# Performance work log

Hardware: AMD Instinct MI355X
Metric: run time of the kernel (lower is better)

## Reference

```python
import jax, jax.numpy as jnp
import numpy as np

N_TRAIN, D, N_EVAL, N_LABELS, K = 100000, 256, 2048, 100, 5


def setup_inputs() -> dict:
    key = jax.random.key(0)
    k1, k2, k3, k4 = jax.random.split(key, 4)
    X_train = jax.random.normal(k1, (N_TRAIN, D), dtype=jnp.float32)
    M = jax.random.normal(k2, (D, D), dtype=jnp.float32)
    X_eval = jax.random.normal(k3, (N_EVAL, D), dtype=jnp.float32)
    y_train = jax.random.randint(k4, (N_TRAIN,), 0, N_LABELS, dtype=jnp.int64 if jax.config.jax_enable_x64 else jnp.int32)
    return {"X_train": X_train, "M": M, "X_eval": X_eval, "y_train": y_train, "n_neighbors": K}


def reference(X_train, M, X_eval, y_train, n_neighbors):
    # cache = X_train @ M (precomputed in the torch module's __init__)
    cache = X_train @ M                                   # [N_train, d]
    X_prod = jnp.sum(cache * X_train, axis=1)             # [N_train]
    Y_prod = jnp.sum((X_eval @ M) * X_eval, axis=1)       # [N_eval]
    cross = cache @ X_eval.T                              # [N_train, N_eval]
    csd = X_prod[:, None] + Y_prod[None, :] - 2.0 * cross # [N_train, N_eval]
    # smallest-k distances per eval point -> top_k of negated distances
    _, indices = jax.lax.top_k(-csd.T, n_neighbors)       # [N_eval, k]
    neighbor_labels = y_train[indices]                    # [N_eval, k]
    n_labels = N_LABELS
    counts = jax.nn.one_hot(neighbor_labels, n_labels, dtype=jnp.float32).sum(axis=1)  # [N_eval, n_labels]
    uniques = jnp.arange(n_labels, dtype=jnp.float32)
    eps = 1.0 / n_labels
    return counts - uniques[None, :] * eps
```

## Files before the change

kernel.cpp:

```cpp
#include <hip/hip_runtime.h>
#include <cfloat>
#include <cstdint>


#define DD    256
#define NLAB  100
#define KNN   5
#define BCOLS 64
#define CHUNK 4224
#define NSRC  8

typedef float4 f4;
typedef __attribute__((ext_vector_type(8))) short bfrag;
typedef __attribute__((ext_vector_type(4))) float f32x4;

__device__ __forceinline__ void gload_lds16(const void* g, void* l) {
  __builtin_amdgcn_global_load_lds(
      (const __attribute__((address_space(1))) void*)g,
      (__attribute__((address_space(3))) void*)l, 16, 0, 0);
}

__device__ __forceinline__ uint32_t hi16(float v) {
  return ((__float_as_uint(v) + 0x8000u) & 0xffff0000u) >> 16;
}

__device__ __forceinline__ void split3(float v, uint32_t& h, uint32_t& m, uint32_t& l) {
  uint32_t b = __float_as_uint(v);
  uint32_t hb = (b + 0x8000u) & 0xffff0000u;
  float r1 = v - __uint_as_float(hb);
  uint32_t b1 = __float_as_uint(r1);
  uint32_t mb = (b1 + 0x8000u) & 0xffff0000u;
  float r2 = r1 - __uint_as_float(mb);
  uint32_t lb = (__float_as_uint(r2) + 0x8000u) & 0xffff0000u;
  h = hb >> 16; m = mb >> 16; l = lb >> 16;
}

__device__ __forceinline__ bool lex_lt(float v, int id, float rv, int rid) {
  return (v < rv) || (v == rv && id < rid);
}

__device__ __forceinline__ void ins5run(float (&bv)[KNN], int (&bi)[KNN], float v, int id) {
  if (v < bv[4]) {
    if (v < bv[3]) {
      bv[4] = bv[3]; bi[4] = bi[3];
      if (v < bv[2]) {
        bv[3] = bv[2]; bi[3] = bi[2];
        if (v < bv[1]) {
          bv[2] = bv[1]; bi[2] = bi[1];
          if (v < bv[0]) {
            bv[1] = bv[0]; bi[1] = bi[0]; bv[0] = v; bi[0] = id;
          } else { bv[1] = v; bi[1] = id; }
        } else { bv[2] = v; bi[2] = id; }
      } else { bv[3] = v; bi[3] = id; }
    } else { bv[4] = v; bi[4] = id; }
  }
}

__device__ __forceinline__ void ins5lex(float (&bv)[KNN], int (&bi)[KNN], float v, int id) {
  if (!lex_lt(v, id, bv[4], bi[4])) return;
  if (lex_lt(v, id, bv[3], bi[3])) {
    bv[4] = bv[3]; bi[4] = bi[3];
    if (lex_lt(v, id, bv[2], bi[2])) {
      bv[3] = bv[2]; bi[3] = bi[2];
      if (lex_lt(v, id, bv[1], bi[1])) {
        bv[2] = bv[1]; bi[2] = bi[1];
        if (lex_lt(v, id, bv[0], bi[0])) {
          bv[1] = bv[0]; bi[1] = bi[0]; bv[0] = v; bi[0] = id;
        } else { bv[1] = v; bi[1] = id; }
      } else { bv[2] = v; bi[2] = id; }
    } else { bv[3] = v; bi[3] = id; }
  } else { bv[4] = v; bi[4] = id; }
}

__device__ __forceinline__ void ins10(float (&bv)[10], int (&bi)[10], float v, int id) {
  if (!lex_lt(v, id, bv[9], bi[9])) return;
  bool placed = false;
#pragma unroll
  for (int s = 9; s >= 1; --s) {
    if (!placed) {
      if (lex_lt(v, id, bv[s - 1], bi[s - 1])) { bv[s] = bv[s - 1]; bi[s] = bi[s - 1]; }
      else { bv[s] = v; bi[s] = id; placed = true; }
    }
  }
  if (!placed) { bv[0] = v; bi[0] = id; }
}

__global__ __launch_bounds__(256)
void msplit_kernel(const float* __restrict__ M, uint4* __restrict__ MT3) {
  int id = blockIdx.x * 256 + threadIdx.x;
  int lane = id & 63;
  int nf = (id >> 6) & 15;
  int kit = id >> 10;
  int d = nf * 16 + (lane & 15);
  int kb = kit * 32 + (lane >> 4) * 8;
  uint32_t hw[4], mw[4], lw[4];
#pragma unroll
  for (int e = 0; e < 4; ++e) {
    uint32_t h0, m0, l0, h1, m1, l1;
    split3(M[(size_t)(kb + 2 * e) * DD + d], h0, m0, l0);
    split3(M[(size_t)(kb + 2 * e + 1) * DD + d], h1, m1, l1);
    hw[e] = h0 | (h1 << 16); mw[e] = m0 | (m1 << 16); lw[e] = l0 | (l1 << 16);
  }
  size_t base = (size_t)(kit * 16 + nf) * 3 * 64;
  MT3[base + lane]       = make_uint4(hw[0], hw[1], hw[2], hw[3]);
  MT3[base + 64 + lane]  = make_uint4(mw[0], mw[1], mw[2], mw[3]);
  MT3[base + 128 + lane] = make_uint4(lw[0], lw[1], lw[2], lw[3]);
}

__global__ __launch_bounds__(256)
void xsplit_kernel(const float* __restrict__ X, uint4* __restrict__ Xsp,
                   int NT, int NT128) {
  int id = blockIdx.x * 256 + threadIdx.x;
  int tile = id >> 12;
  if (tile >= NT128) return;
  int rem = id & 4095;
  int kit = rem >> 10;
  int s = rem & 1023;
  int m = s >> 3, pos = s & 7;
  int jj = pos ^ (m & 7);
  int row = tile * 128 + m; if (row >= NT) row = NT - 1;
  const float* src = X + (size_t)row * DD + kit * 64 + jj * 8;
  f4 v0 = *(const f4*)src;
  f4 v1 = *(const f4*)(src + 4);
  uint32_t h0 = hi16(v0.x) | (hi16(v0.y) << 16);
  uint32_t h1 = hi16(v0.z) | (hi16(v0.w) << 16);
  uint32_t h2 = hi16(v1.x) | (hi16(v1.y) << 16);
  uint32_t h3 = hi16(v1.z) | (hi16(v1.w) << 16);
  Xsp[(((size_t)tile * 4 + kit) << 10) + s] = make_uint4(h0, h1, h2, h3);
}

__global__ __launch_bounds__(256)
void prep_kernel(const float* __restrict__ M, const float* __restrict__ Xe,
                 float* __restrict__ ZTf32, uint4* __restrict__ Z2h, int NEVAL) {
  __shared__ float xe_lds[64 * 257];
  const int t = threadIdx.x;
  const int j0 = blockIdx.x * 64;
  const int part = t >> 6;
  const int dbase = blockIdx.y * 64 + part * 16;
#pragma unroll
  for (int it = 0; it < 16; ++it) {
    int id = t + it * 256;
    int r = id >> 6, k4 = id & 63;
    f4 v = *(const f4*)(Xe + (size_t)(j0 + r) * DD + 4 * k4);
    float* p = &xe_lds[r * 257 + 4 * k4];
    p[0] = v.x; p[1] = v.y; p[2] = v.z; p[3] = v.w;
  }
  __syncthreads();
  const int j = t & 63;
  float acc[16];
#pragma unroll
  for (int dd = 0; dd < 16; ++dd) acc[dd] = 0.f;
  for (int k4 = 0; k4 < 64; ++k4) {
    const float* xp = &xe_lds[j * 257 + 4 * k4];
    float x0 = xp[0], x1 = xp[1], x2 = xp[2], x3 = xp[3];
#pragma unroll
    for (int dd = 0; dd < 16; ++dd) {
      f4 m = *(const f4*)(M + (size_t)(dbase + dd) * DD + 4 * k4);
      acc[dd] = fmaf(m.x, x0, fmaf(m.y, x1, fmaf(m.z, x2, fmaf(m.w, x3, acc[dd]))));
    }
  }
  const int jg = j0 + j;
#pragma unroll
  for (int dd = 0; dd < 16; ++dd)
    ZTf32[(size_t)(dbase + dd) * NEVAL + jg] = acc[dd];
  const int cc = jg & 63, ct2 = jg >> 6;
  const int kit64 = dbase >> 6;
  const int jb = (dbase & 63) >> 3;
  size_t zbase = (size_t)ct2 * 2048 + kit64 * 512 + cc * 8;
#pragma unroll
  for (int u = 0; u < 2; ++u) {
    int jj = jb + u;
    uint32_t hw[4];
#pragma unroll
    for (int e = 0; e < 4; ++e) {
      uint32_t a0 = hi16(-2.f * acc[u * 8 + 2 * e]);
      uint32_t a1 = hi16(-2.f * acc[u * 8 + 2 * e + 1]);
      hw[e] = a0 | (a1 << 16);
    }
    Z2h[zbase + (jj ^ (cc & 7))] = make_uint4(hw[0], hw[1], hw[2], hw[3]);
  }
}

__global__ __launch_bounds__(256, 2)
void xprod_kernel(const float* __restrict__ X, const uint4* __restrict__ MT3,
                  float* __restrict__ Xprod, int NT) {
  __shared__ __align__(16) char pool[66560];
  short* A3 = (short*)pool;
  char*  B3 = pool + 12288;
  float* C  = (float*)pool;

  const int t = threadIdx.x;
  const int w = t >> 6, lane = t & 63;
  const int l15 = lane & 15, l4 = lane >> 4;
  const int row0 = blockIdx.x * 64;
  const int r = t >> 2, g = t & 3;
  int grow = row0 + r; if (grow >= NT) grow = NT - 1;
  const float* xrow = X + (size_t)grow * DD;

  f32x4 acc[16];
#pragma unroll
  for (int nf = 0; nf < 16; ++nf) { f32x4 z = {0.f, 0.f, 0.f, 0.f}; acc[nf] = z; }

  for (int kit = 0; kit < 8; ++kit) {
    f4 v0 = *(const f4*)(xrow + kit * 32 + g * 8);
    f4 v1 = *(const f4*)(xrow + kit * 32 + g * 8 + 4);
    uint32_t h[8], m[8], l[8];
    split3(v0.x, h[0], m[0], l[0]); split3(v0.y, h[1], m[1], l[1]);
    split3(v0.z, h[2], m[2], l[2]); split3(v0.w, h[3], m[3], l[3]);
    split3(v1.x, h[4], m[4], l[4]); split3(v1.y, h[5], m[5], l[5]);
    split3(v1.z, h[6], m[6], l[6]); split3(v1.w, h[7], m[7], l[7]);
    int slot = (r & 15) + 16 * g;
    int wb = r >> 4;
    *(uint4*)((char*)A3 + ((wb * 3 + 0) * 64 + slot) * 16) =
        make_uint4(h[0] | (h[1] << 16), h[2] | (h[3] << 16), h[4] | (h[5] << 16), h[6] | (h[7] << 16));
    *(uint4*)((char*)A3 + ((wb * 3 + 1) * 64 + slot) * 16) =
        make_uint4(m[0] | (m[1] << 16), m[2] | (m[3] << 16), m[4] | (m[5] << 16), m[6] | (m[7] << 16));
    *(uint4*)((char*)A3 + ((wb * 3 + 2) * 64 + slot) * 16) =
        make_uint4(l[0] | (l[1] << 16), l[2] | (l[3] << 16), l[4] | (l[5] << 16), l[6] | (l[7] << 16));
    const uint4* src = MT3 + (size_t)kit * 3072;
#pragma unroll
    for (int i = 0; i < 12; ++i) {
      int gs = (w * 12 + i) * 64;
      gload_lds16(src + gs + lane, B3 + (size_t)gs * 16);
    }
    __syncthreads();
    bfrag ah = *(const bfrag*)((const char*)A3 + ((w * 3 + 0) * 64 + lane) * 16);
    bfrag am = *(const bfrag*)((const char*)A3 + ((w * 3 + 1) * 64 + lane) * 16);
    bfrag al = *(const bfrag*)((const char*)A3 + ((w * 3 + 2) * 64 + lane) * 16);
#pragma unroll
    for (int nf = 0; nf < 16; ++nf) {
      bfrag bh = *(const bfrag*)(B3 + ((nf * 3 + 0) * 64 + lane) * 16);
      bfrag bm = *(const bfrag*)(B3 + ((nf * 3 + 1) * 64 + lane) * 16);
      bfrag bl = *(const bfrag*)(B3 + ((nf * 3 + 2) * 64 + lane) * 16);
      acc[nf] = __builtin_amdgcn_mfma_f32_16x16x32_bf16(ah, bh, acc[nf], 0, 0, 0);
      acc[nf] = __builtin_amdgcn_mfma_f32_16x16x32_bf16(ah, bm, acc[nf], 0, 0, 0);
      acc[nf] = __builtin_amdgcn_mfma_f32_16x16x32_bf16(am, bh, acc[nf], 0, 0, 0);
      acc[nf] = __builtin_amdgcn_mfma_f32_16x16x32_bf16(ah, bl, acc[nf], 0, 0, 0);
      acc[nf] = __builtin_amdgcn_mfma_f32_16x16x32_bf16(al, bh, acc[nf], 0, 0, 0);
      acc[nf] = __builtin_amdgcn_mfma_f32_16x16x32_bf16(am, bm, acc[nf], 0, 0, 0);
    }
    __syncthreads();
  }
#pragma unroll
  for (int nf = 0; nf < 16; ++nf)
#pragma unroll
    for (int reg = 0; reg < 4; ++reg)
      C[(size_t)(16 * w + l4 * 4 + reg) * 260 + nf * 16 + l15] = acc[nf][reg];
  __syncthreads();
  float part = 0.f;
#pragma unroll
  for (int j = 0; j < 16; ++j) {
    f4 xv = *(const f4*)(xrow + g * 64 + 4 * j);
    f4 cv = *(const f4*)&C[(size_t)r * 260 + g * 64 + 4 * j];
    part = fmaf(xv.x, cv.x, fmaf(xv.y, cv.y, fmaf(xv.z, cv.z, fmaf(xv.w, cv.w, part))));
  }
  part += __shfl_xor(part, 1);
  part += __shfl_xor(part, 2);
  if (g == 0 && row0 + r < NT) Xprod[row0 + r] = part;
}

__global__ __launch_bounds__(256, 3)
void cross_topk_kernel(const uint4* __restrict__ Xsp, const uint4* __restrict__ Z2h,
                       const float* __restrict__ Xprod,
                       float* __restrict__ cand_v, int* __restrict__ cand_i,
                       int NT, int NCH, int NT128) {
  __shared__ __align__(16) char Abuf[2][16384];
  __shared__ __align__(16) char Bbuf[2][8192];
  __shared__ __align__(16) float xp_lds[256];

  const int t = threadIdx.x;
  const int w = t >> 6, lane = t & 63;
  const int l15 = lane & 15, l4 = lane >> 4;
  const int wr = (w & 1) * 64;
  const int wc = (w >> 1) * 32;
  int n = blockIdx.y * gridDim.x + blockIdx.x;
  int nwg = gridDim.x * gridDim.y;
  int wg = n;
  if ((nwg & 7) == 0) wg = (n & 7) * (nwg >> 3) + (n >> 3);
  const int ct = wg % gridDim.x;
  const int ch = wg / gridDim.x;
  const int c0 = ct * BCOLS;
  const int row0 = ch * CHUNK;
  const int rows = min(CHUNK, NT - row0);
  const int nrp = (rows + 127) >> 7;
  const int G = nrp * 4;
  const int tile0 = ch * (CHUNK >> 7);

  float bv[2][KNN]; int bi[2][KNN];
#pragma unroll
  for (int nf = 0; nf < 2; ++nf)
#pragma unroll
    for (int s = 0; s < KNN; ++s) { bv[nf][s] = FLT_MAX; bi[nf][s] = 0x7fffffff; }

  f32x4 acc[4][2];
#pragma unroll
  for (int mf = 0; mf < 4; ++mf)
#pragma unroll
    for (int nf = 0; nf < 2; ++nf) { f32x4 z = {0.f, 0.f, 0.f, 0.f}; acc[mf][nf] = z; }

  auto stageA = [&](int gg) {
    int tile = tile0 + (gg >> 2); if (tile >= NT128) tile = NT128 - 1;
    const uint4* src = Xsp + (((size_t)tile * 4 + (gg & 3)) << 10);
    char* dst = Abuf[gg & 1];
#pragma unroll
    for (int i = 0; i < 4; ++i) {
      int sb = (w * 4 + i) * 64;
      gload_lds16(src + sb + lane, dst + sb * 16);
    }
  };
  auto stageB = [&](int gg) {
    const uint4* src = Z2h + (size_t)ct * 2048 + (gg & 3) * 512;
    char* dst = Bbuf[gg & 1];
#pragma unroll
    for (int i = 0; i < 2; ++i) {
      int sb = (w * 2 + i) * 64;
      gload_lds16(src + sb + lane, dst + sb * 16);
    }
  };

  stageA(0); stageB(0);
  asm volatile("s_waitcnt vmcnt(0)" ::: "memory");
  __builtin_amdgcn_s_barrier();

  for (int rp = 0; rp < nrp; ++rp) {
#pragma unroll
    for (int kit = 0; kit < 4; ++kit) {
      const int g = rp * 4 + kit;
      if (g < G - 1) {
        stageA(g + 1); stageB(g + 1);
        if (kit == 0 && !(rp & 1)) {
          gload_lds16((const uint4*)(Xprod + row0 + rp * 128) + lane,
                      (char*)xp_lds);
        }
        asm volatile("s_waitcnt vmcnt(3)" ::: "memory");
      } else {
        asm volatile("s_waitcnt vmcnt(0)" ::: "memory");
      }
      __builtin_amdgcn_s_barrier();
      const char* Ab = Abuf[kit & 1];
      const char* Bb = Bbuf[kit & 1];
      bfrag ah[4][2], bh[2][2];
#pragma unroll
      for (int mf = 0; mf < 4; ++mf) {
        int m = wr + mf * 16 + l15;
        const char* rb = Ab + m * 128;
#pragma unroll
        for (int ks = 0; ks < 2; ++ks)
          ah[mf][ks] = *(const bfrag*)(rb + (((ks * 4 + l4) ^ (m & 7)) << 4));
      }
#pragma unroll
      for (int nf = 0; nf < 2; ++nf) {
        int cc = wc + nf * 16 + l15;
        const char* rb = Bb + cc * 128;
#pragma unroll
        for (int ks = 0; ks < 2; ++ks)
          bh[nf][ks] = *(const bfrag*)(rb + (((ks * 4 + l4) ^ (cc & 7)) << 4));
      }
      __builtin_amdgcn_s_setprio(1);
#pragma unroll
      for (int ks = 0; ks < 2; ++ks)
#pragma unroll
        for (int mf = 0; mf < 4; ++mf)
#pragma unroll
          for (int nf = 0; nf < 2; ++nf)
            acc[mf][nf] = __builtin_amdgcn_mfma_f32_16x16x32_bf16(
                ah[mf][ks], bh[nf][ks], acc[mf][nf], 0, 0, 0);
      __builtin_amdgcn_s_setprio(0);
      if (kit == 3) {
        const int trow0 = row0 + rp * 128;
        const bool full = (trow0 + 128 <= NT);
#pragma unroll
        for (int mf = 0; mf < 4; ++mf) {
          f4 xv = *(const f4*)&xp_lds[(rp & 1) * 128 + wr + mf * 16 + l4 * 4];
          const int rbase = trow0 + wr + mf * 16 + l4 * 4;
#pragma unroll
          for (int nf = 0; nf < 2; ++nf) {
            float v0 = xv.x + acc[mf][nf][0];
            float v1 = xv.y + acc[mf][nf][1];
            float v2 = xv.z + acc[mf][nf][2];
            float v3 = xv.w + acc[mf][nf][3];
            if (!full) {
              if (rbase + 0 >= NT) v0 = FLT_MAX;
              if (rbase + 1 >= NT) v1 = FLT_MAX;
              if (rbase + 2 >= NT) v2 = FLT_MAX;
              if (rbase + 3 >= NT) v3 = FLT_MAX;
            }
            float mn = fminf(fminf(v0, v1), fminf(v2, v3));
            if (mn < bv[nf][4]) {
              ins5run(bv[nf], bi[nf], v0, rbase);
              ins5run(bv[nf], bi[nf], v1, rbase + 1);
              ins5run(bv[nf], bi[nf], v2, rbase + 2);
              ins5run(bv[nf], bi[nf], v3, rbase + 3);
            }
            f32x4 zz = {0.f, 0.f, 0.f, 0.f};
            acc[mf][nf] = zz;
          }
        }
      }
      __builtin_amdgcn_s_barrier();
    }
  }

#pragma unroll
  for (int nf = 0; nf < 2; ++nf) {
    int col = c0 + wc + nf * 16 + l15;
    size_t o = ((size_t)col * NCH + ch) * (NSRC * KNN) + ((w & 1) * 4 + l4) * KNN;
#pragma unroll
    for (int s = 0; s < KNN; ++s) { cand_v[o + s] = bv[nf][s]; cand_i[o + s] = bi[nf][s]; }
  }
}

__global__ __launch_bounds__(64)
void finalize_kernel(const float* __restrict__ cand_v, const int* __restrict__ cand_i,
                     const float* __restrict__ X, const float* __restrict__ ZTf32,
                     const float* __restrict__ Xprod, const int* __restrict__ y,
                     float* __restrict__ out, int NCH, int NEVAL, int NT) {
  __shared__ float ztl[DD];
  const int j = blockIdx.x;
  const int lane = threadIdx.x;
#pragma unroll
  for (int i = 0; i < 4; ++i) {
    int k = lane + 64 * i;
    ztl[k] = ZTf32[(size_t)k * NEVAL + j];
  }
  __syncthreads();

  float bv[10]; int bi[10];
#pragma unroll
  for (int s = 0; s < 10; ++s) { bv[s] = FLT_MAX; bi[s] = 0x7fffffff; }
  const int NC = NCH * NSRC * KNN;
  const float* cvj = cand_v + (size_t)j * NC;
  const int*   cij = cand_i + (size_t)j * NC;
  for (int p = lane; p < NC; p += 64)
    ins10(bv, bi, cvj[p], cij[p]);
#pragma unroll
  for (int st = 0; st < 6; ++st) {
    float pv[10]; int pi[10];
#pragma unroll
    for (int s = 0; s < 10; ++s) {
      pv[s] = __shfl_xor(bv[s], 1 << st);
      pi[s] = __shfl_xor(bi[s], 1 << st);
    }
#pragma unroll
    for (int s = 0; s < 10; ++s) ins10(bv, bi, pv[s], pi[s]);
  }
  float ex[10];
#pragma unroll
  for (int c = 0; c < 10; ++c) {
    int idx = bi[c];
    float part = 0.f;
#pragma unroll
    for (int i = 0; i < 4; ++i) {
      int k = lane + 64 * i;
      part = fmaf(X[(size_t)idx * DD + k], ztl[k], part);
    }
#pragma unroll
    for (int st = 0; st < 6; ++st) part += __shfl_xor(part, 1 << st);
    ex[c] = Xprod[idx] - 2.f * part;
  }
  float fv[KNN]; int fi[KNN];
#pragma unroll
  for (int s = 0; s < KNN; ++s) { fv[s] = FLT_MAX; fi[s] = 0x7fffffff; }
#pragma unroll
  for (int c = 0; c < 10; ++c) ins5lex(fv, fi, ex[c], bi[c]);
  int lb[KNN];
#pragma unroll
  for (int s = 0; s < KNN; ++s) lb[s] = y[fi[s]];
  for (int q = lane; q < NLAB; q += 64) {
    int cnt = (lb[0] == q) + (lb[1] == q) + (lb[2] == q) + (lb[3] == q) + (lb[4] == q);
    out[(size_t)j * NLAB + q] = (float)cnt - (float)q * 0.01f;
  }
}

extern "C" void kernel_launch(void* const* d_in, const int* in_sizes, int n_in,
                              void* d_out, int out_size, void* d_ws, size_t ws_size,
                              hipStream_t stream) {
  const float* X  = (const float*)d_in[0];
  const float* M  = (const float*)d_in[1];
  const float* Xe = (const float*)d_in[2];
  const int*   y  = (const int*)d_in[3];
  const int NT    = in_sizes[0] / DD;
  const int NEVAL = in_sizes[2] / DD;
  const int NCH   = (NT + CHUNK - 1) / CHUNK;
  const int NT64  = (NT + 63) / 64;
  const int NT128 = (NT + 127) / 128;

  char* ws = (char*)d_ws;
  uint4* Z2h    = (uint4*)ws;
  float* ZTf32  = (float*)(ws + (1 << 20));
  uint4* MT3    = (uint4*)(ws + (3 << 20));
  float* Xprod  = (float*)(ws + (3 << 20) + (448 << 10));
  float* cand_v = (float*)(ws + (4 << 20));
  int*   cand_i = (int*)(cand_v + (size_t)NEVAL * NCH * NSRC * KNN);
  uint4* Xsp    = (uint4*)(ws + (40ULL << 20));
  float* out    = (float*)d_out;

  msplit_kernel<<<dim3(32), 256, 0, stream>>>(M, MT3);
  prep_kernel<<<dim3(NEVAL / 64, DD / 64), 256, 0, stream>>>(M, Xe, ZTf32, Z2h, NEVAL);
  xsplit_kernel<<<dim3(NT128 * 16), 256, 0, stream>>>(X, Xsp, NT, NT128);
  xprod_kernel<<<dim3(NT64), 256, 0, stream>>>(X, MT3, Xprod, NT);
  cross_topk_kernel<<<dim3(NEVAL / BCOLS, NCH), 256, 0, stream>>>(
      Xsp, Z2h, Xprod, cand_v, cand_i, NT, NCH, NT128);
  finalize_kernel<<<dim3(NEVAL), 64, 0, stream>>>(
      cand_v, cand_i, X, ZTf32, Xprod, y, out, NCH, NEVAL, NT);
}
```

Before: 399.8 us.

## Halve the K-step per stage in cross_topk to shrink LDS and raise occupancy

Re-lays out the bf16 Xsp and Z2h buffers into 32-wide K slices with a new swizzle, and changes the cross_topk pipeline to eight K-steps per row tile instead of four. This halves the A and B LDS double buffers, which allows four workgroups per CU instead of three. CHUNK is also roughly halved, so there are more row chunks and more workgroups in flight. In exchange there are twice as many barriers and smaller loads per K-step, and the downstream merge has more per-chunk candidates to combine.

```diff
diff --git a/kernel.cpp b/kernel.cpp
--- a/kernel.cpp
+++ b/kernel.cpp
@@ -7,7 +7,7 @@
 #define NLAB  100
 #define KNN   5
 #define BCOLS 64
-#define CHUNK 4224
+#define CHUNK 2176
 #define NSRC  8
 
 typedef float4 f4;
@@ -114,19 +114,19 @@
   int tile = id >> 12;
   if (tile >= NT128) return;
   int rem = id & 4095;
-  int kit = rem >> 10;
-  int s = rem & 1023;
-  int m = s >> 3, pos = s & 7;
-  int jj = pos ^ (m & 7);
+  int kit32 = rem >> 9;
+  int s = rem & 511;
+  int m = s >> 2, qs = s & 3;
+  int q = qs ^ ((m >> 1) & 3);
   int row = tile * 128 + m; if (row >= NT) row = NT - 1;
-  const float* src = X + (size_t)row * DD + kit * 64 + jj * 8;
+  const float* src = X + (size_t)row * DD + kit32 * 32 + q * 8;
   f4 v0 = *(const f4*)src;
   f4 v1 = *(const f4*)(src + 4);
   uint32_t h0 = hi16(v0.x) | (hi16(v0.y) << 16);
   uint32_t h1 = hi16(v0.z) | (hi16(v0.w) << 16);
   uint32_t h2 = hi16(v1.x) | (hi16(v1.y) << 16);
   uint32_t h3 = hi16(v1.z) | (hi16(v1.w) << 16);
-  Xsp[(((size_t)tile * 4 + kit) << 10) + s] = make_uint4(h0, h1, h2, h3);
+  Xsp[id] = make_uint4(h0, h1, h2, h3);
 }
 
 __global__ __launch_bounds__(256)
@@ -164,12 +164,11 @@
   for (int dd = 0; dd < 16; ++dd)
     ZTf32[(size_t)(dbase + dd) * NEVAL + jg] = acc[dd];
   const int cc = jg & 63, ct2 = jg >> 6;
-  const int kit64 = dbase >> 6;
-  const int jb = (dbase & 63) >> 3;
-  size_t zbase = (size_t)ct2 * 2048 + kit64 * 512 + cc * 8;
+  const int kit32 = dbase >> 5;
+  const int oqb = (dbase & 31) >> 3;
+  size_t zbase = ((size_t)ct2 * 8 + kit32) * 256 + cc * 4;
 #pragma unroll
   for (int u = 0; u < 2; ++u) {
-    int jj = jb + u;
     uint32_t hw[4];
 #pragma unroll
     for (int e = 0; e < 4; ++e) {
@@ -177,7 +176,8 @@
       uint32_t a1 = hi16(-2.f * acc[u * 8 + 2 * e + 1]);
       hw[e] = a0 | (a1 << 16);
     }
-    Z2h[zbase + (jj ^ (cc & 7))] = make_uint4(hw[0], hw[1], hw[2], hw[3]);
+    Z2h[zbase + ((oqb + u) ^ ((cc >> 1) & 3))] =
+        make_uint4(hw[0], hw[1], hw[2], hw[3]);
   }
 }
 
@@ -259,13 +259,13 @@
   if (g == 0 && row0 + r < NT) Xprod[row0 + r] = part;
 }
 
-__global__ __launch_bounds__(256, 3)
+__global__ __launch_bounds__(256, 4)
 void cross_topk_kernel(const uint4* __restrict__ Xsp, const uint4* __restrict__ Z2h,
                        const float* __restrict__ Xprod,
                        float* __restrict__ cand_v, int* __restrict__ cand_i,
                        int NT, int NCH, int NT128) {
-  __shared__ __align__(16) char Abuf[2][16384];
-  __shared__ __align__(16) char Bbuf[2][8192];
+  __shared__ __align__(16) char Abuf[2][8192];
+  __shared__ __align__(16) char Bbuf[2][4096];
   __shared__ __align__(16) float xp_lds[256];
 
   const int t = threadIdx.x;
@@ -283,7 +283,7 @@
   const int row0 = ch * CHUNK;
   const int rows = min(CHUNK, NT - row0);
   const int nrp = (rows + 127) >> 7;
-  const int G = nrp * 4;
+  const int G = nrp * 8;
   const int tile0 = ch * (CHUNK >> 7);
 
   float bv[2][KNN]; int bi[2][KNN];
@@ -299,24 +299,19 @@
     for (int nf = 0; nf < 2; ++nf) { f32x4 z = {0.f, 0.f, 0.f, 0.f}; acc[mf][nf] = z; }
 
   auto stageA = [&](int gg) {
-    int tile = tile0 + (gg >> 2); if (tile >= NT128) tile = NT128 - 1;
-    const uint4* src = Xsp + (((size_t)tile * 4 + (gg & 3)) << 10);
+    int tile = tile0 + (gg >> 3); if (tile >= NT128) tile = NT128 - 1;
+    const uint4* src = Xsp + (((size_t)tile * 8 + (gg & 7)) << 9);
     char* dst = Abuf[gg & 1];
-#pragma unroll
-    for (int i = 0; i < 4; ++i) {
-      int sb = (w * 4 + i) * 64;
-      gload_lds16(src + sb + lane, dst + sb * 16);
-    }
-  };
-  auto stageB = [&](int gg) {
-    const uint4* src = Z2h + (size_t)ct * 2048 + (gg & 3) * 512;
-    char* dst = Bbuf[gg & 1];
 #pragma unroll
     for (int i = 0; i < 2; ++i) {
       int sb = (w * 2 + i) * 64;
       gload_lds16(src + sb + lane, dst + sb * 16);
     }
   };
+  auto stageB = [&](int gg) {
+    const uint4* src = Z2h + ((size_t)ct * 8 + (gg & 7)) * 256;
+    gload_lds16(src + w * 64 + lane, Bbuf[gg & 1] + (w * 64) * 16);
+  };
 
   stageA(0); stageB(0);
   asm volatile("s_waitcnt vmcnt(0)" ::: "memory");
@@ -324,8 +319,8 @@
 
   for (int rp = 0; rp < nrp; ++rp) {
 #pragma unroll
-    for (int kit = 0; kit < 4; ++kit) {
-      const int g = rp * 4 + kit;
+    for (int kit = 0; kit < 8; ++kit) {
+      const int g = rp * 8 + kit;
       if (g < G - 1) {
         stageA(g + 1); stageB(g + 1);
         if (kit == 0 && !(rp & 1)) {
@@ -339,34 +334,26 @@
       __builtin_amdgcn_s_barrier();
       const char* Ab = Abuf[kit & 1];
       const char* Bb = Bbuf[kit & 1];
-      bfrag ah[4][2], bh[2][2];
+      bfrag ah[4], bh[2];
 #pragma unroll
       for (int mf = 0; mf < 4; ++mf) {
         int m = wr + mf * 16 + l15;
-        const char* rb = Ab + m * 128;
-#pragma unroll
-        for (int ks = 0; ks < 2; ++ks)
-          ah[mf][ks] = *(const bfrag*)(rb + (((ks * 4 + l4) ^ (m & 7)) << 4));
+        ah[mf] = *(const bfrag*)(Ab + m * 64 + ((l4 ^ ((m >> 1) & 3)) << 4));
       }
 #pragma unroll
       for (int nf = 0; nf < 2; ++nf) {
         int cc = wc + nf * 16 + l15;
-        const char* rb = Bb + cc * 128;
-#pragma unroll
-        for (int ks = 0; ks < 2; ++ks)
-          bh[nf][ks] = *(const bfrag*)(rb + (((ks * 4 + l4) ^ (cc & 7)) << 4));
+        bh[nf] = *(const bfrag*)(Bb + cc * 64 + ((l4 ^ ((cc >> 1) & 3)) << 4));
       }
       __builtin_amdgcn_s_setprio(1);
 #pragma unroll
-      for (int ks = 0; ks < 2; ++ks)
-#pragma unroll
-        for (int mf = 0; mf < 4; ++mf)
-#pragma unroll
-          for (int nf = 0; nf < 2; ++nf)
-            acc[mf][nf] = __builtin_amdgcn_mfma_f32_16x16x32_bf16(
-                ah[mf][ks], bh[nf][ks], acc[mf][nf], 0, 0, 0);
+      for (int mf = 0; mf < 4; ++mf)
+#pragma unroll
+        for (int nf = 0; nf < 2; ++nf)
+          acc[mf][nf] = __builtin_amdgcn_mfma_f32_16x16x32_bf16(
+              ah[mf], bh[nf], acc[mf][nf], 0, 0, 0);
       __builtin_amdgcn_s_setprio(0);
-      if (kit == 3) {
+      if (kit == 7) {
         const int trow0 = row0 + rp * 128;
         const bool full = (trow0 + 128 <= NT);
 #pragma unroll
```

After: 458.1 us. +14.6%, slower.

## Use two-term bf16 split for X@M and fuse X bf16 packing into xprod

Applied to the files above, without the earlier changes.

Splits fp32 operands into two bf16 terms (high, truncated low) instead of three, so X@M needs 3 MFMAs per fragment instead of 6 and moves less LDS and global traffic for M. The separate xsplit kernel is removed, and xprod_kernel now writes the swizzled bf16 high parts of X into Xsp as a side effect. This saves one pass over X_train and one launch. The cost is lower accuracy in Xprod, which could change near-tie neighbor selection, though finalize may recheck candidates in fp32.

```diff
diff --git a/kernel.cpp b/kernel.cpp
--- a/kernel.cpp
+++ b/kernel.cpp
@@ -24,15 +24,12 @@
   return ((__float_as_uint(v) + 0x8000u) & 0xffff0000u) >> 16;
 }
 
-__device__ __forceinline__ void split3(float v, uint32_t& h, uint32_t& m, uint32_t& l) {
+__device__ __forceinline__ void split2(float v, uint32_t& h, uint32_t& l) {
   uint32_t b = __float_as_uint(v);
   uint32_t hb = (b + 0x8000u) & 0xffff0000u;
-  float r1 = v - __uint_as_float(hb);
-  uint32_t b1 = __float_as_uint(r1);
-  uint32_t mb = (b1 + 0x8000u) & 0xffff0000u;
-  float r2 = r1 - __uint_as_float(mb);
-  uint32_t lb = (__float_as_uint(r2) + 0x8000u) & 0xffff0000u;
-  h = hb >> 16; m = mb >> 16; l = lb >> 16;
+  float lf = v - __uint_as_float(hb);
+  h = hb >> 16;
+  l = __float_as_uint(lf) >> 16;
 }
 
 __device__ __forceinline__ bool lex_lt(float v, int id, float rv, int rid) {
@@ -86,47 +83,24 @@
 }
 
 __global__ __launch_bounds__(256)
-void msplit_kernel(const float* __restrict__ M, uint4* __restrict__ MT3) {
+void msplit_kernel(const float* __restrict__ M, uint4* __restrict__ MT2) {
   int id = blockIdx.x * 256 + threadIdx.x;
   int lane = id & 63;
   int nf = (id >> 6) & 15;
   int kit = id >> 10;
   int d = nf * 16 + (lane & 15);
   int kb = kit * 32 + (lane >> 4) * 8;
-  uint32_t hw[4], mw[4], lw[4];
+  uint32_t hw[4], lw[4];
 #pragma unroll
   for (int e = 0; e < 4; ++e) {
-    uint32_t h0, m0, l0, h1, m1, l1;
-    split3(M[(size_t)(kb + 2 * e) * DD + d], h0, m0, l0);
-    split3(M[(size_t)(kb + 2 * e + 1) * DD + d], h1, m1, l1);
-    hw[e] = h0 | (h1 << 16); mw[e] = m0 | (m1 << 16); lw[e] = l0 | (l1 << 16);
-  }
-  size_t base = (size_t)(kit * 16 + nf) * 3 * 64;
-  MT3[base + lane]       = make_uint4(hw[0], hw[1], hw[2], hw[3]);
-  MT3[base + 64 + lane]  = make_uint4(mw[0], mw[1], mw[2], mw[3]);
-  MT3[base + 128 + lane] = make_uint4(lw[0], lw[1], lw[2], lw[3]);
-}
-
-__global__ __launch_bounds__(256)
-void xsplit_kernel(const float* __restrict__ X, uint4* __restrict__ Xsp,
-                   int NT, int NT128) {
-  int id = blockIdx.x * 256 + threadIdx.x;
-  int tile = id >> 12;
-  if (tile >= NT128) return;
-  int rem = id & 4095;
-  int kit = rem >> 10;
-  int s = rem & 1023;
-  int m = s >> 3, pos = s & 7;
-  int jj = pos ^ (m & 7);
-  int row = tile * 128 + m; if (row >= NT) row = NT - 1;
-  const float* src = X + (size_t)row * DD + kit * 64 + jj * 8;
-  f4 v0 = *(const f4*)src;
-  f4 v1 = *(const f4*)(src + 4);
-  uint32_t h0 = hi16(v0.x) | (hi16(v0.y) << 16);
-  uint32_t h1 = hi16(v0.z) | (hi16(v0.w) << 16);
-  uint32_t h2 = hi16(v1.x) | (hi16(v1.y) << 16);
-  uint32_t h3 = hi16(v1.z) | (hi16(v1.w) << 16);
-  Xsp[(((size_t)tile * 4 + kit) << 10) + s] = make_uint4(h0, h1, h2, h3);
+    uint32_t h0, l0, h1, l1;
+    split2(M[(size_t)(kb + 2 * e) * DD + d], h0, l0);
+    split2(M[(size_t)(kb + 2 * e + 1) * DD + d], h1, l1);
+    hw[e] = h0 | (h1 << 16); lw[e] = l0 | (l1 << 16);
+  }
+  size_t base = (size_t)(kit * 16 + nf) * 2 * 64;
+  MT2[base + lane]      = make_uint4(hw[0], hw[1], hw[2], hw[3]);
+  MT2[base + 64 + lane] = make_uint4(lw[0], lw[1], lw[2], lw[3]);
 }
 
 __global__ __launch_bounds__(256)
@@ -182,11 +156,11 @@
 }
 
 __global__ __launch_bounds__(256, 2)
-void xprod_kernel(const float* __restrict__ X, const uint4* __restrict__ MT3,
-                  float* __restrict__ Xprod, int NT) {
+void xprod_kernel(const float* __restrict__ X, const uint4* __restrict__ MT2,
+                  float* __restrict__ Xprod, uint4* __restrict__ Xsp, int NT) {
   __shared__ __align__(16) char pool[66560];
-  short* A3 = (short*)pool;
-  char*  B3 = pool + 12288;
+  short* A2 = (short*)pool;
+  char*  B2 = pool + 8192;
   float* C  = (float*)pool;
 
   const int t = threadIdx.x;
@@ -194,8 +168,10 @@
   const int l15 = lane & 15, l4 = lane >> 4;
   const int row0 = blockIdx.x * 64;
   const int r = t >> 2, g = t & 3;
-  int grow = row0 + r; if (grow >= NT) grow = NT - 1;
+  const int rowid = row0 + r;
+  int grow = rowid; if (grow >= NT) grow = NT - 1;
   const float* xrow = X + (size_t)grow * DD;
+  const int xm = rowid & 127, xtile = rowid >> 7;
 
   f32x4 acc[16];
 #pragma unroll
@@ -204,40 +180,39 @@
   for (int kit = 0; kit < 8; ++kit) {
     f4 v0 = *(const f4*)(xrow + kit * 32 + g * 8);
     f4 v1 = *(const f4*)(xrow + kit * 32 + g * 8 + 4);
-    uint32_t h[8], m[8], l[8];
-    split3(v0.x, h[0], m[0], l[0]); split3(v0.y, h[1], m[1], l[1]);
-    split3(v0.z, h[2], m[2], l[2]); split3(v0.w, h[3], m[3], l[3]);
-    split3(v1.x, h[4], m[4], l[4]); split3(v1.y, h[5], m[5], l[5]);
-    split3(v1.z, h[6], m[6], l[6]); split3(v1.w, h[7], m[7], l[7]);
+    uint32_t h[8], l[8];
+    split2(v0.x, h[0], l[0]); split2(v0.y, h[1], l[1]);
+    split2(v0.z, h[2], l[2]); split2(v0.w, h[3], l[3]);
+    split2(v1.x, h[4], l[4]); split2(v1.y, h[5], l[5]);
+    split2(v1.z, h[6], l[6]); split2(v1.w, h[7], l[7]);
+    uint4 hp = make_uint4(h[0] | (h[1] << 16), h[2] | (h[3] << 16),
+                          h[4] | (h[5] << 16), h[6] | (h[7] << 16));
+    {
+      int jj = (kit & 1) * 4 + g;
+      Xsp[(((size_t)xtile * 4 + (kit >> 1)) << 10) + xm * 8 + (jj ^ (xm & 7))] = hp;
+    }
     int slot = (r & 15) + 16 * g;
     int wb = r >> 4;
-    *(uint4*)((char*)A3 + ((wb * 3 + 0) * 64 + slot) * 16) =
-        make_uint4(h[0] | (h[1] << 16), h[2] | (h[3] << 16), h[4] | (h[5] << 16), h[6] | (h[7] << 16));
-    *(uint4*)((char*)A3 + ((wb * 3 + 1) * 64 + slot) * 16) =
-        make_uint4(m[0] | (m[1] << 16), m[2] | (m[3] << 16), m[4] | (m[5] << 16), m[6] | (m[7] << 16));
-    *(uint4*)((char*)A3 + ((wb * 3 + 2) * 64 + slot) * 16) =
-        make_uint4(l[0] | (l[1] << 16), l[2] | (l[3] << 16), l[4] | (l[5] << 16), l[6] | (l[7] << 16));
-    const uint4* src = MT3 + (size_t)kit * 3072;
-#pragma unroll
-    for (int i = 0; i < 12; ++i) {
-      int gs = (w * 12 + i) * 64;
-      gload_lds16(src + gs + lane, B3 + (size_t)gs * 16);
+    *(uint4*)((char*)A2 + ((wb * 2 + 0) * 64 + slot) * 16) = hp;
+    *(uint4*)((char*)A2 + ((wb * 2 + 1) * 64 + slot) * 16) =
+        make_uint4(l[0] | (l[1] << 16), l[2] | (l[3] << 16),
+                   l[4] | (l[5] << 16), l[6] | (l[7] << 16));
+    const uint4* src = MT2 + (size_t)kit * 2048;
+#pragma unroll
+    for (int i = 0; i < 8; ++i) {
+      int gs = (w * 8 + i) * 64;
+      gload_lds16(src + gs + lane, B2 + (size_t)gs * 16);
     }
     __syncthreads();
-    bfrag ah = *(const bfrag*)((const char*)A3 + ((w * 3 + 0) * 64 + lane) * 16);
-    bfrag am = *(const bfrag*)((const char*)A3 + ((w * 3 + 1) * 64 + lane) * 16);
-    bfrag al = *(const bfrag*)((const char*)A3 + ((w * 3 + 2) * 64 + lane) * 16);
+    bfrag ah = *(const bfrag*)((const char*)A2 + ((w * 2 + 0) * 64 + lane) * 16);
+    bfrag al = *(const bfrag*)((const char*)A2 + ((w * 2 + 1) * 64 + lane) * 16);
 #pragma unroll
     for (int nf = 0; nf < 16; ++nf) {
-      bfrag bh = *(const bfrag*)(B3 + ((nf * 3 + 0) * 64 + lane) * 16);
-      bfrag bm = *(const bfrag*)(B3 + ((nf * 3 + 1) * 64 + lane) * 16);
-      bfrag bl = *(const bfrag*)(B3 + ((nf * 3 + 2) * 64 + lane) * 16);
+      bfrag bh = *(const bfrag*)(B2 + ((nf * 2 + 0) * 64 + lane) * 16);
+      bfrag bl = *(const bfrag*)(B2 + ((nf * 2 + 1) * 64 + lane) * 16);
       acc[nf] = __builtin_amdgcn_mfma_f32_16x16x32_bf16(ah, bh, acc[nf], 0, 0, 0);
-      acc[nf] = __builtin_amdgcn_mfma_f32_16x16x32_bf16(ah, bm, acc[nf], 0, 0, 0);
-      acc[nf] = __builtin_amdgcn_mfma_f32_16x16x32_bf16(am, bh, acc[nf], 0, 0, 0);
       acc[nf] = __builtin_amdgcn_mfma_f32_16x16x32_bf16(ah, bl, acc[nf], 0, 0, 0);
       acc[nf] = __builtin_amdgcn_mfma_f32_16x16x32_bf16(al, bh, acc[nf], 0, 0, 0);
-      acc[nf] = __builtin_amdgcn_mfma_f32_16x16x32_bf16(am, bm, acc[nf], 0, 0, 0);
     }
     __syncthreads();
   }
@@ -256,7 +231,7 @@
   }
   part += __shfl_xor(part, 1);
   part += __shfl_xor(part, 2);
-  if (g == 0 && row0 + r < NT) Xprod[row0 + r] = part;
+  if (g == 0 && rowid < NT) Xprod[rowid] = part;
 }
 
 __global__ __launch_bounds__(256, 3)
@@ -488,17 +463,16 @@
   char* ws = (char*)d_ws;
   uint4* Z2h    = (uint4*)ws;
   float* ZTf32  = (float*)(ws + (1 << 20));
-  uint4* MT3    = (uint4*)(ws + (3 << 20));
+  uint4* MT2    = (uint4*)(ws + (3 << 20));
   float* Xprod  = (float*)(ws + (3 << 20) + (448 << 10));
   float* cand_v = (float*)(ws + (4 << 20));
   int*   cand_i = (int*)(cand_v + (size_t)NEVAL * NCH * NSRC * KNN);
   uint4* Xsp    = (uint4*)(ws + (40ULL << 20));
   float* out    = (float*)d_out;
 
-  msplit_kernel<<<dim3(32), 256, 0, stream>>>(M, MT3);
+  msplit_kernel<<<dim3(32), 256, 0, stream>>>(M, MT2);
   prep_kernel<<<dim3(NEVAL / 64, DD / 64), 256, 0, stream>>>(M, Xe, ZTf32, Z2h, NEVAL);
-  xsplit_kernel<<<dim3(NT128 * 16), 256, 0, stream>>>(X, Xsp, NT, NT128);
-  xprod_kernel<<<dim3(NT64), 256, 0, stream>>>(X, MT3, Xprod, NT);
+  xprod_kernel<<<dim3(NT64), 256, 0, stream>>>(X, MT2, Xprod, Xsp, NT);
   cross_topk_kernel<<<dim3(NEVAL / BCOLS, NCH), 256, 0, stream>>>(
       Xsp, Z2h, Xprod, cand_v, cand_i, NT, NCH, NT128);
   finalize_kernel<<<dim3(NEVAL), 64, 0, stream>>>(
```

Result: faster. 356.9 us (-10.7%).
